# Performance work log

Measured on AMD Instinct MI355X. Metric: run time of the kernel, lower is better.

## Reference

```python
import jax, jax.numpy as jnp
import numpy as np

N = 50000      # nodes
E = 800000     # edges
F_IN = 16      # feature_size
D = 96         # d_model
G = 64         # graphs per batch


def _gcn_conv(x, W, b, src, dst, dis, num_nodes):
    # PyG GCNConv: out = D^{-1/2}(A+I)D^{-1/2} X W + b (self-loops already in src/dst)
    h = x @ W                                   # [N, out]
    norm = (dis[src] * dis[dst])[:, None]       # [E+N, 1]
    msg = h[src] * norm                         # gather + scale
    agg = jax.ops.segment_sum(msg, dst, num_segments=num_nodes)
    return agg + b


def _forward(x, W_init, b_init, W1, b1, W2, b2, W3, b3, W4, b4,
             Wo1, bo1, Wo2, bo2, edge_index, batch_index):
    act = jax.nn.leaky_relu  # default negative_slope=0.01, matches nn.LeakyReLU()
    n = x.shape[0]
    # add self-loops once; degree includes self-loop (PyG gcn_norm default)
    loop = jnp.arange(n, dtype=edge_index.dtype)
    src = jnp.concatenate([edge_index[0], loop])
    dst = jnp.concatenate([edge_index[1], loop])
    deg = jax.ops.segment_sum(jnp.ones_like(src, dtype=x.dtype), dst, num_segments=n)
    dis = jax.lax.rsqrt(deg)  # deg >= 1 due to self-loops

    h = act(_gcn_conv(x, W_init, b_init, src, dst, dis, n))
    h = act(_gcn_conv(h, W1, b1, src, dst, dis, n))
    h = act(_gcn_conv(h, W2, b2, src, dst, dis, n))
    h = act(_gcn_conv(h, W3, b3, src, dst, dis, n))
    h = act(_gcn_conv(h, W4, b4, src, dst, dis, n))

    # global max + mean pooling per graph
    gmax = jax.ops.segment_max(h, batch_index, num_segments=G)
    gsum = jax.ops.segment_sum(h, batch_index, num_segments=G)
    cnt = jax.ops.segment_sum(jnp.ones((n,), dtype=h.dtype), batch_index, num_segments=G)
    gmean = gsum / jnp.maximum(cnt, 1.0)[:, None]
    pooled = jnp.concatenate([gmax, gmean], axis=1)  # [G, 2D]

    out = act(pooled @ Wo1 + bo1)  # dropout is identity in eval
    out = out @ Wo2 + bo2          # [G, 1]
    return out


def setup_inputs() -> dict:
    key = jax.random.key(0)
    ks = jax.random.split(key, 16)
    def glorot(k, shape):
        lim = float(np.sqrt(6.0 / (shape[0] + shape[1])))
        return jax.random.uniform(k, shape, jnp.float32, -lim, lim)
    inp = {
        'x': jax.random.normal(ks[0], (N, F_IN), jnp.float32),
        'edge_index': jax.random.randint(ks[1], (2, E), 0, N, dtype=jnp.int64),
        'batch_index': jnp.sort(jax.random.randint(ks[2], (N,), 0, G, dtype=jnp.int64)),
        'W_init': glorot(ks[3], (F_IN, D)), 'b_init': jnp.zeros((D,), jnp.float32),
        'W1': glorot(ks[4], (D, D)), 'b1': jnp.zeros((D,), jnp.float32),
        'W2': glorot(ks[5], (D, D)), 'b2': jnp.zeros((D,), jnp.float32),
        'W3': glorot(ks[6], (D, D)), 'b3': jnp.zeros((D,), jnp.float32),
        'W4': glorot(ks[7], (D, D)), 'b4': jnp.zeros((D,), jnp.float32),
        'Wo1': glorot(ks[8], (2 * D, D)), 'bo1': jnp.zeros((D,), jnp.float32),
        'Wo2': glorot(ks[9], (D, 1)), 'bo2': jnp.zeros((1,), jnp.float32),
    }
    return inp


def reference(x, edge_index, batch_index, W_init, b_init, W1, b1, W2, b2,
              W3, b3, W4, b4, Wo1, bo1, Wo2, bo2):
    return _forward(x, W_init, b_init, W1, b1, W2, b2, W3, b3, W4, b4,
                    Wo1, bo1, Wo2, bo2, edge_index, batch_index)
```

## Files before the change

kernel.cpp:

```cpp
#include <hip/hip_runtime.h>
#include <hip/hip_fp16.h>
#include <math.h>

#define LEAKY(x) ((x) > 0.f ? (x) : 0.01f * (x))
#define BK_SHIFT 9
#define NBMAX 128
#define BCAP 16384

typedef _Float16 half8 __attribute__((ext_vector_type(8)));
typedef float f32x4 __attribute__((ext_vector_type(4)));

__device__ __forceinline__ void add4(float4& acc, const float4& v) {
    acc.x += v.x; acc.y += v.y; acc.z += v.z; acc.w += v.w;
}

#define FMIX_LO(acc, u, one) \
    asm("v_fma_mix_f32 %0, %1, %2, %0 op_sel:[0,0,0] op_sel_hi:[1,0,0]" \
        : "+v"(acc) : "v"(u), "v"(one))
#define FMIX_HI(acc, u, one) \
    asm("v_fma_mix_f32 %0, %1, %2, %0 op_sel:[1,0,0] op_sel_hi:[1,0,0]" \
        : "+v"(acc) : "v"(u), "v"(one))

__device__ __forceinline__ unsigned encf(float f) {
    unsigned u = __float_as_uint(f);
    return (u & 0x80000000u) ? ~u : (u | 0x80000000u);
}
__device__ __forceinline__ float decf(unsigned u) {
    if (u == 0u) return -INFINITY;
    unsigned b = (u & 0x80000000u) ? (u & 0x7fffffffu) : ~u;
    return __uint_as_float(b);
}

__global__ __launch_bounds__(256) void prep(const float* __restrict__ W1,
                                            const float* __restrict__ W2,
                                            const float* __restrict__ W3,
                                            const float* __restrict__ W4,
                                            _Float16* __restrict__ WtG,
                                            int* __restrict__ bfill,
                                            unsigned* __restrict__ gmaxU,
                                            float* __restrict__ gsum, int G) {
    int bi = blockIdx.x, tid = threadIdx.x;
    if (bi < 4) {
        const float* W = bi == 0 ? W1 : bi == 1 ? W2 : bi == 2 ? W3 : W4;
        _Float16* dst = WtG + bi * 9216;
        for (int idx = tid; idx < 9216; idx += 256) {
            int k = idx / 96, nn = idx % 96;
            dst[nn * 96 + k] = (_Float16)W[idx];
        }
    } else if (bi == 4) {
        for (int i2 = tid; i2 < NBMAX; i2 += 256) bfill[i2] = 0;
    } else if (bi == 5) {
        for (int i2 = tid; i2 < G * 96; i2 += 256) gmaxU[i2] = 0u;
    } else {
        for (int i2 = tid; i2 < G * 96; i2 += 256) gsum[i2] = 0.f;
    }
}

__global__ __launch_bounds__(256) void bin_kernel(const int* __restrict__ src,
                                                  const int* __restrict__ dst,
                                                  int* __restrict__ bfill,
                                                  uint2* __restrict__ tmp,
                                                  int E, int nb) {
    __shared__ int hist[NBMAX];
    __shared__ int scanbuf[NBMAX];
    __shared__ int lofs[NBMAX];
    __shared__ int adj[NBMAX];
    __shared__ uint2 buf[2048];
    __shared__ unsigned char bkt_of[2048];
    int base = blockIdx.x * 2048;
    int cnt = min(2048, E - base);
    int tid = threadIdx.x;
    for (int b = tid; b < NBMAX; b += 256) hist[b] = 0;
    __syncthreads();
    int es[8], ed[8];
#pragma unroll
    for (int k = 0; k < 8; ++k) {
        int l = tid + k * 256;
        if (l < cnt) {
            es[k] = src[base + l];
            ed[k] = dst[base + l];
            atomicAdd(&hist[ed[k] >> BK_SHIFT], 1);
        }
    }
    __syncthreads();
    if (tid < NBMAX) scanbuf[tid] = hist[tid];
    __syncthreads();
    for (int off = 1; off < NBMAX; off <<= 1) {
        int t = (tid < NBMAX && tid >= off) ? scanbuf[tid - off] : 0;
        __syncthreads();
        if (tid < NBMAX) scanbuf[tid] += t;
        __syncthreads();
    }
    if (tid < nb) {
        int cb = hist[tid];
        int start = scanbuf[tid] - cb;
        lofs[tid] = start;
        int g = (cb > 0) ? atomicAdd(&bfill[tid], cb) : 0;
        adj[tid] = tid * BCAP + g - start;
    }
    __syncthreads();
#pragma unroll
    for (int k = 0; k < 8; ++k) {
        int l = tid + k * 256;
        if (l < cnt) {
            int b = ed[k] >> BK_SHIFT;
            int r = atomicAdd(&lofs[b], 1);
            buf[r] = make_uint2((unsigned)es[k], (unsigned)ed[k]);
            bkt_of[r] = (unsigned char)b;
        }
    }
    __syncthreads();
    for (int j = tid; j < cnt; j += 256) {
        int b = bkt_of[j];
        tmp[adj[b] + j] = buf[j];
    }
}

__global__ __launch_bounds__(512) void place2(const uint2* __restrict__ tmp,
                                              const int* __restrict__ bfill,
                                              const float* __restrict__ X,
                                              float* __restrict__ dis,
                                              int* __restrict__ row_ptr,
                                              int* __restrict__ edge_src,
                                              float* __restrict__ Z0, int kq,
                                              int n, int E, int nb) {
    __shared__ int hist[512];
    __shared__ int sc[512];
    __shared__ int sbf[NBMAX];
    __shared__ int bb_s;
    int b = blockIdx.x;
    int tid = threadIdx.x;
    if (tid < NBMAX) sbf[tid] = (tid < nb) ? bfill[tid] : 0;
    hist[tid] = 0;
    __syncthreads();
    if (tid == 0) {
        int s = 0;
        for (int k = 0; k < b; ++k) s += sbf[k];
        bb_s = s;
    }
    __syncthreads();
    int bb = bb_s;
    int cnt = sbf[b];
    const uint2* mybkt = tmp + (size_t)b * BCAP;
    int node0 = b << BK_SHIFT;
    for (int j = tid; j < cnt; j += 512)
        atomicAdd(&hist[(int)mybkt[j].y - node0], 1);
    __syncthreads();
    int v = hist[tid];
    sc[tid] = v;
    __syncthreads();
    for (int off = 1; off < 512; off <<= 1) {
        int t = (tid >= off) ? sc[tid - off] : 0;
        __syncthreads();
        sc[tid] += t;
        __syncthreads();
    }
    int excl = sc[tid] - v;
    int i = node0 + tid;
    if (i < n) {
        row_ptr[i] = bb + excl;
        float di = rsqrtf((float)(v + 1));
        dis[i] = di;
        const float4* X4 = (const float4*)X;
        float4* Z4 = (float4*)Z0;
        for (int j = 0; j < kq; ++j) {
            float4 xv = X4[(size_t)i * kq + j];
            Z4[(size_t)i * kq + j] = make_float4(di * xv.x, di * xv.y, di * xv.z, di * xv.w);
        }
    }
    if (b == 0 && tid == 0) row_ptr[n] = E;
    __syncthreads();
    hist[tid] = bb + excl;
    __syncthreads();
    for (int j = tid; j < cnt; j += 512) {
        uint2 ev = mybkt[j];
        int pos = atomicAdd(&hist[(int)ev.y - node0], 1);
        edge_src[pos] = (int)ev.x;
    }
}

template <int LPN, int F4PL, int UNROLL>
__global__ __launch_bounds__(256) void agg_wave(const float* __restrict__ Z,
                                                const float* __restrict__ dis,
                                                const int* __restrict__ row_ptr,
                                                const int* __restrict__ edge_src,
                                                float* __restrict__ A, int n) {
    constexpr int GROUPS = 64 / LPN;
    constexpr int KQ = LPN * F4PL;
    int i = (blockIdx.x * 256 + threadIdx.x) >> 6;
    if (i >= n) return;
    int lane = threadIdx.x & 63;
    int g = lane / LPN;
    int c = lane % LPN;
    const float4* Z4 = (const float4*)Z;
    float di = dis[i];
    size_t base = (size_t)i * KQ + c * F4PL;
    float4 acc[F4PL];
    if (g == 0) {
#pragma unroll
        for (int j = 0; j < F4PL; ++j) acc[j] = Z4[base + j];
    } else {
#pragma unroll
        for (int j = 0; j < F4PL; ++j) acc[j] = make_float4(0.f, 0.f, 0.f, 0.f);
    }
    int re0 = row_ptr[i], re1 = row_ptr[i + 1];
#pragma unroll UNROLL
    for (int e = re0 + g; e < re1; e += GROUPS) {
        int s = edge_src[e];
        size_t sb = (size_t)s * KQ + c * F4PL;
#pragma unroll
        for (int j = 0; j < F4PL; ++j) {
            float4 xs = Z4[sb + j];
            add4(acc[j], xs);
        }
    }
#pragma unroll
    for (int m = LPN; m < 64; m <<= 1) {
#pragma unroll
        for (int j = 0; j < F4PL; ++j) {
            acc[j].x += __shfl_xor(acc[j].x, m);
            acc[j].y += __shfl_xor(acc[j].y, m);
            acc[j].z += __shfl_xor(acc[j].z, m);
            acc[j].w += __shfl_xor(acc[j].w, m);
        }
    }
    if (g == 0) {
#pragma unroll
        for (int j = 0; j < F4PL; ++j) {
            float4 o = make_float4(di * acc[j].x, di * acc[j].y,
                                   di * acc[j].z, di * acc[j].w);
            ((float4*)A)[base + j] = o;
        }
    }
}

__global__ __launch_bounds__(256) void agg_wave_h(const __half* __restrict__ Zh,
                                                  const float* __restrict__ dis,
                                                  const int* __restrict__ row_ptr,
                                                  const int* __restrict__ edge_src,
                                                  __half* __restrict__ A, int n) {
    int i = (blockIdx.x * 256 + threadIdx.x) >> 6;
    if (i >= n) return;
    int lane = threadIdx.x & 63;
    int g = lane >> 3;
    int c = lane & 7;
    float di = dis[i];
    float one = 1.0f;
    float acc[12];
#pragma unroll
    for (int k = 0; k < 12; ++k) acc[k] = 0.f;
    if (g == 0) {
        const uint2* zp = (const uint2*)(Zh + (size_t)i * 96 + c * 12);
        uint2 u0 = zp[0], u1 = zp[1], u2 = zp[2];
        FMIX_LO(acc[0], u0.x, one); FMIX_HI(acc[1], u0.x, one);
        FMIX_LO(acc[2], u0.y, one); FMIX_HI(acc[3], u0.y, one);
        FMIX_LO(acc[4], u1.x, one); FMIX_HI(acc[5], u1.x, one);
        FMIX_LO(acc[6], u1.y, one); FMIX_HI(acc[7], u1.y, one);
        FMIX_LO(acc[8], u2.x, one); FMIX_HI(acc[9], u2.x, one);
        FMIX_LO(acc[10], u2.y, one); FMIX_HI(acc[11], u2.y, one);
    }
    int re0 = row_ptr[i], re1 = row_ptr[i + 1];
#pragma unroll 4
    for (int e = re0 + g; e < re1; e += 8) {
        int s = __builtin_nontemporal_load(&edge_src[e]);
        const uint2* zp = (const uint2*)(Zh + (size_t)s * 96 + c * 12);
        uint2 u0 = zp[0], u1 = zp[1], u2 = zp[2];
        FMIX_LO(acc[0], u0.x, one); FMIX_HI(acc[1], u0.x, one);
        FMIX_LO(acc[2], u0.y, one); FMIX_HI(acc[3], u0.y, one);
        FMIX_LO(acc[4], u1.x, one); FMIX_HI(acc[5], u1.x, one);
        FMIX_LO(acc[6], u1.y, one); FMIX_HI(acc[7], u1.y, one);
        FMIX_LO(acc[8], u2.x, one); FMIX_HI(acc[9], u2.x, one);
        FMIX_LO(acc[10], u2.y, one); FMIX_HI(acc[11], u2.y, one);
    }
#pragma unroll
    for (int m = 8; m < 64; m <<= 1) {
#pragma unroll
        for (int k = 0; k < 12; ++k) acc[k] += __shfl_xor(acc[k], m);
    }
    if (g == 0) {
        __half2 h0 = __floats2half2_rn(di * acc[0], di * acc[1]);
        __half2 h1 = __floats2half2_rn(di * acc[2], di * acc[3]);
        __half2 h2 = __floats2half2_rn(di * acc[4], di * acc[5]);
        __half2 h3 = __floats2half2_rn(di * acc[6], di * acc[7]);
        __half2 h4 = __floats2half2_rn(di * acc[8], di * acc[9]);
        __half2 h5 = __floats2half2_rn(di * acc[10], di * acc[11]);
        uint2 o0, o1, o2;
        o0.x = *(unsigned*)&h0; o0.y = *(unsigned*)&h1;
        o1.x = *(unsigned*)&h2; o1.y = *(unsigned*)&h3;
        o2.x = *(unsigned*)&h4; o2.y = *(unsigned*)&h5;
        uint2* ap = (uint2*)(A + (size_t)i * 96 + c * 12);
        ap[0] = o0; ap[1] = o1; ap[2] = o2;
    }
}

template <bool SCALE>
__global__ __launch_bounds__(256) void gemm_mfma(const __half* __restrict__ A,
                                                 const _Float16* __restrict__ Wt,
                                                 const float* __restrict__ b,
                                                 const float* __restrict__ dis,
                                                 __half* __restrict__ Xn, int n) {
    int tid = threadIdx.x;
    int i0 = blockIdx.x * 64;
    int w = tid >> 6, lane = tid & 63;
    int q = lane >> 4, c = lane & 15;
    int arow = i0 + w * 16 + c;
    const _Float16* Ap = (const _Float16*)A;
    half8 af[3];
    if (arow < n) {
#pragma unroll
        for (int kc = 0; kc < 3; ++kc)
            af[kc] = *(const half8*)&Ap[(size_t)arow * 96 + kc * 32 + q * 8];
    } else {
#pragma unroll
        for (int kc = 0; kc < 3; ++kc)
#pragma unroll
            for (int j = 0; j < 8; ++j) af[kc][j] = (_Float16)0.f;
    }
    float dvals[4];
#pragma unroll
    for (int r = 0; r < 4; ++r) {
        int gi = i0 + w * 16 + q * 4 + r;
        dvals[r] = (SCALE && gi < n) ? dis[gi] : 1.f;
    }
#pragma unroll
    for (int nt = 0; nt < 6; ++nt) {
        f32x4 acc = {0.f, 0.f, 0.f, 0.f};
#pragma unroll
        for (int kc = 0; kc < 3; ++kc) {
            half8 bf = *(const half8*)&Wt[(size_t)(nt * 16 + c) * 96 + kc * 32 + q * 8];
            acc = __builtin_amdgcn_mfma_f32_16x16x32_f16(af[kc], bf, acc, 0, 0, 0);
        }
        int col = nt * 16 + c;
        float bias = b[col];
#pragma unroll
        for (int r = 0; r < 4; ++r) {
            int gi = i0 + w * 16 + q * 4 + r;
            if (gi < n) {
                float v = acc[r] + bias;
                v = LEAKY(v);
                if (SCALE) v *= dvals[r];
                ((_Float16*)Xn)[(size_t)gi * 96 + col] = (_Float16)v;
            }
        }
    }
}

__global__ __launch_bounds__(256) void gemm_pool(const __half* __restrict__ A,
                                                 const _Float16* __restrict__ Wt,
                                                 const float* __restrict__ b,
                                                 const int* __restrict__ batch,
                                                 unsigned* __restrict__ gmaxU,
                                                 float* __restrict__ gsum, int n) {
    __shared__ float pmaxs[4][96];
    __shared__ float psums[4][96];
    int tid = threadIdx.x;
    int i0 = blockIdx.x * 64;
    int w = tid >> 6, lane = tid & 63;
    int q = lane >> 4, c = lane & 15;
    int arow = i0 + w * 16 + c;
    const _Float16* Ap = (const _Float16*)A;
    half8 af[3];
    if (arow < n) {
#pragma unroll
        for (int kc = 0; kc < 3; ++kc)
            af[kc] = *(const half8*)&Ap[(size_t)arow * 96 + kc * 32 + q * 8];
    } else {
#pragma unroll
        for (int kc = 0; kc < 3; ++kc)
#pragma unroll
            for (int j = 0; j < 8; ++j) af[kc][j] = (_Float16)0.f;
    }
    int row0 = i0 + w * 16;
    bool wuni = (row0 + 15 < n) && (batch[row0] == batch[row0 + 15]);
    bool buni = (i0 + 63 < n) && (batch[i0] == batch[i0 + 63]);
    int gw = wuni ? batch[row0] : 0;
#pragma unroll
    for (int nt = 0; nt < 6; ++nt) {
        f32x4 acc = {0.f, 0.f, 0.f, 0.f};
#pragma unroll
        for (int kc = 0; kc < 3; ++kc) {
            half8 bf = *(const half8*)&Wt[(size_t)(nt * 16 + c) * 96 + kc * 32 + q * 8];
            acc = __builtin_amdgcn_mfma_f32_16x16x32_f16(af[kc], bf, acc, 0, 0, 0);
        }
        int col = nt * 16 + c;
        float bias = b[col];
        float v[4];
#pragma unroll
        for (int r = 0; r < 4; ++r) {
            float t = acc[r] + bias;
            v[r] = LEAKY(t);
        }
        if (wuni) {
            float mx = fmaxf(fmaxf(v[0], v[1]), fmaxf(v[2], v[3]));
            float sm = v[0] + v[1] + v[2] + v[3];
            mx = fmaxf(mx, __shfl_xor(mx, 16)); sm += __shfl_xor(sm, 16);
            mx = fmaxf(mx, __shfl_xor(mx, 32)); sm += __shfl_xor(sm, 32);
            if (buni) {
                if (q == 0) { pmaxs[w][col] = mx; psums[w][col] = sm; }
            } else if (q == 0) {
                atomicMax(&gmaxU[gw * 96 + col], encf(mx));
                atomicAdd(&gsum[gw * 96 + col], sm);
            }
        } else {
            int r = 0;
            while (r < 4) {
                int gi = i0 + w * 16 + q * 4 + r;
                if (gi >= n) break;
                int gb = batch[gi];
                float mx = v[r], sm = v[r];
                int r2 = r + 1;
                for (; r2 < 4; ++r2) {
                    int gi2 = i0 + w * 16 + q * 4 + r2;
                    if (gi2 >= n || batch[gi2] != gb) break;
                    mx = fmaxf(mx, v[r2]); sm += v[r2];
                }
                atomicMax(&gmaxU[gb * 96 + col], encf(mx));
                atomicAdd(&gsum[gb * 96 + col], sm);
                r = r2;
            }
        }
    }
    __syncthreads();
    if (buni && tid < 96) {
        float m = fmaxf(fmaxf(pmaxs[0][tid], pmaxs[1][tid]),
                        fmaxf(pmaxs[2][tid], pmaxs[3][tid]));
        float s = psums[0][tid] + psums[1][tid] + psums[2][tid] + psums[3][tid];
        int gb = batch[i0];
        atomicMax(&gmaxU[gb * 96 + tid], encf(m));
        atomicAdd(&gsum[gb * 96 + tid], s);
    }
}

__global__ __launch_bounds__(192) void gemm_l0(const float* __restrict__ A,
                                               const float* __restrict__ W,
                                               const float* __restrict__ b,
                                               const float* __restrict__ dis,
                                               __half* __restrict__ Xn, int n) {
    constexpr int KQ = 4;
    __shared__ __align__(16) float4 Al[64 * KQ];
    int tid = threadIdx.x;
    int i0 = blockIdx.x * 64;
    for (int idx = tid; idx < 64 * KQ; idx += 192) {
        int gi = i0 + idx / KQ;
        Al[idx] = (gi < n) ? ((const float4*)A)[(size_t)i0 * KQ + idx]
                           : make_float4(0.f, 0.f, 0.f, 0.f);
    }
    __syncthreads();
    int fq = tid % 24;
    int g = tid / 24;
    const float4* W4 = (const float4*)W;
    float4 bb = ((const float4*)b)[fq];
    float4 acc[8];
#pragma unroll
    for (int r = 0; r < 8; ++r) acc[r] = bb;
    for (int kc = 0; kc < 16; kc += 8) {
        float4 w[8];
#pragma unroll
        for (int kk = 0; kk < 8; ++kk) w[kk] = W4[(size_t)(kc + kk) * 24 + fq];
#pragma unroll
        for (int r = 0; r < 8; ++r) {
            const float4* ar = &Al[(g * 8 + r) * KQ + (kc >> 2)];
#pragma unroll
            for (int k4 = 0; k4 < 2; ++k4) {
                float4 a = ar[k4];
                float4 w0 = w[4 * k4 + 0], w1 = w[4 * k4 + 1];
                float4 w2 = w[4 * k4 + 2], w3 = w[4 * k4 + 3];
                acc[r].x += a.x * w0.x + a.y * w1.x + a.z * w2.x + a.w * w3.x;
                acc[r].y += a.x * w0.y + a.y * w1.y + a.z * w2.y + a.w * w3.y;
                acc[r].z += a.x * w0.z + a.y * w1.z + a.z * w2.z + a.w * w3.z;
                acc[r].w += a.x * w0.w + a.y * w1.w + a.z * w2.w + a.w * w3.w;
            }
        }
    }
#pragma unroll
    for (int r = 0; r < 8; ++r) {
        int gi = i0 + g * 8 + r;
        if (gi < n) {
            float di = dis[gi];
            float4 o;
            o.x = di * LEAKY(acc[r].x); o.y = di * LEAKY(acc[r].y);
            o.z = di * LEAKY(acc[r].z); o.w = di * LEAKY(acc[r].w);
            __half2 h0 = __floats2half2_rn(o.x, o.y);
            __half2 h1 = __floats2half2_rn(o.z, o.w);
            uint2 u;
            u.x = *(unsigned*)&h0;
            u.y = *(unsigned*)&h1;
            ((uint2*)Xn)[(size_t)gi * 24 + fq] = u;
        }
    }
}

__device__ __forceinline__ int lower_bound(const int* b, int n, int v) {
    int lo = 0, hi = n;
    while (lo < hi) {
        int m = (lo + hi) >> 1;
        if (b[m] < v) lo = m + 1; else hi = m;
    }
    return lo;
}

__global__ void pool_final(const unsigned* __restrict__ gmaxU,
                           const float* __restrict__ gsum,
                           const int* __restrict__ batch,
                           const float* __restrict__ Wo1, const float* __restrict__ bo1,
                           const float* __restrict__ Wo2, const float* __restrict__ bo2,
                           float* __restrict__ out, int n) {
    __shared__ float pooled[192];
    __shared__ float sh[96];
    int g = blockIdx.x, f = threadIdx.x;
    int s = lower_bound(batch, n, g), e = lower_bound(batch, n, g + 1);
    float cnt = fmaxf((float)(e - s), 1.f);
    pooled[f] = decf(gmaxU[(size_t)g * 96 + f]);
    pooled[96 + f] = gsum[(size_t)g * 96 + f] / cnt;
    __syncthreads();
    float acc = bo1[f];
    for (int k = 0; k < 192; ++k) acc += pooled[k] * Wo1[k * 96 + f];
    float a = LEAKY(acc);
    sh[f] = a * Wo2[f];
    __syncthreads();
    if (f == 0) {
        float sacc = 0.f;
        for (int k = 0; k < 96; ++k) sacc += sh[k];
        out[g] = sacc + bo2[0];
    }
}

extern "C" void kernel_launch(void* const* d_in, const int* in_sizes, int n_in,
                              void* d_out, int out_size, void* d_ws, size_t ws_size,
                              hipStream_t stream) {
    const float* x      = (const float*)d_in[0];
    const int*   eidx   = (const int*)d_in[1];
    const int*   batch  = (const int*)d_in[2];
    const float* W_init = (const float*)d_in[3];
    const float* b_init = (const float*)d_in[4];
    const float* W1 = (const float*)d_in[5];  const float* b1 = (const float*)d_in[6];
    const float* W2 = (const float*)d_in[7];  const float* b2 = (const float*)d_in[8];
    const float* W3 = (const float*)d_in[9];  const float* b3 = (const float*)d_in[10];
    const float* W4 = (const float*)d_in[11]; const float* b4 = (const float*)d_in[12];
    const float* Wo1 = (const float*)d_in[13]; const float* bo1 = (const float*)d_in[14];
    const float* Wo2 = (const float*)d_in[15]; const float* bo2 = (const float*)d_in[16];
    float* out = (float*)d_out;

    const int N = in_sizes[2];
    const int E = in_sizes[1] / 2;
    const int G = out_size;
    const int* src = eidx;
    const int* dst = eidx + E;

    const int nbBkt  = (N + (1 << BK_SHIFT) - 1) >> BK_SHIFT;

    char* ws = (char*)d_ws;
    size_t off = 0;
    auto alloc = [&](size_t bytes) {
        size_t o = off;
        off += (bytes + 255) & ~(size_t)255;
        return o;
    };
    float*    dis      = (float*)(ws + alloc((size_t)N * 4));
    int*      row_ptr  = (int*)(ws + alloc((size_t)(N + 1) * 4));
    int*      bfill    = (int*)(ws + alloc(NBMAX * 4));
    unsigned* gmaxU    = (unsigned*)(ws + alloc((size_t)G * 96 * 4));
    float*    gsumB    = (float*)(ws + alloc((size_t)G * 96 * 4));
    int*      edge_src = (int*)(ws + alloc((size_t)E * 4));
    float*    Z0       = (float*)(ws + alloc((size_t)N * 16 * 4));
    __half*   ZA       = (__half*)(ws + alloc((size_t)N * 96 * 2));
    __half*   ZB       = (__half*)(ws + alloc((size_t)N * 96 * 2));
    __half*   AggH     = (__half*)(ws + alloc((size_t)N * 96 * 2));
    float*    Agg0     = (float*)(ws + alloc((size_t)N * 16 * 4));
    _Float16* WtG      = (_Float16*)(ws + alloc((size_t)4 * 9216 * 2));
    uint2*    tmp      = (uint2*)(ws + alloc((size_t)nbBkt * BCAP * 8));
    (void)ws_size; (void)n_in;

    const int nbWave = (N + 3) / 4;
    const int nbTile = (N + 63) / 64;

    prep<<<7, 256, 0, stream>>>(W1, W2, W3, W4, WtG, bfill, gmaxU, gsumB, G);
    bin_kernel<<<(E + 2047) / 2048, 256, 0, stream>>>(src, dst, bfill, tmp, E, nbBkt);
    place2<<<nbBkt, 512, 0, stream>>>(tmp, bfill, x, dis, row_ptr, edge_src, Z0,
                                      4, N, E, nbBkt);

    agg_wave<4, 1, 2><<<nbWave, 256, 0, stream>>>(Z0, dis, row_ptr, edge_src, Agg0, N);
    gemm_l0<<<nbTile, 192, 0, stream>>>(Agg0, W_init, b_init, dis, ZA, N);

    const float* bs[4] = {b1, b2, b3, b4};
    __half* cur = ZA;
    __half* nxt = ZB;
    for (int l = 0; l < 4; ++l) {
        agg_wave_h<<<nbWave, 256, 0, stream>>>(cur, dis, row_ptr, edge_src, AggH, N);
        if (l < 3) {
            gemm_mfma<true><<<nbTile, 256, 0, stream>>>(AggH, WtG + l * 9216, bs[l],
                                                        dis, nxt, N);
            __half* t = cur; cur = nxt; nxt = t;
        } else {
            gemm_pool<<<nbTile, 256, 0, stream>>>(AggH, WtG + 3 * 9216, bs[3],
                                                  batch, gmaxU, gsumB, N);
        }
    }

    pool_final<<<G, 96, 0, stream>>>(gmaxU, gsumB, batch, Wo1, bo1, Wo2, bo2, out, N);
}
```

Measured before the change: 344.6 us.

## Fuse neighbor aggregation into the MFMA GEMM kernels for hidden layers

Replaces the separate wave-per-node aggregation kernel and the following MFMA GEMM (or GEMM+pool) kernel with one templated kernel. In it, each lane accumulates its node's neighbor features directly in the MFMA A-fragment layout, with four lanes per node walking the edge list serially. The aggregated, scaled fp16 fragment then feeds the MFMA without an intermediate buffer. This removes one launch per layer and the write and re-read of the N×96 aggregation buffer, but cuts per-node parallelism from 8 edge groups to a serial loop per lane and lowers total wave count, which may expose gather latency.

```diff
diff --git a/kernel.cpp b/kernel.cpp
--- a/kernel.cpp
+++ b/kernel.cpp
@@ -20,6 +20,23 @@
 #define FMIX_HI(acc, u, one) \
     asm("v_fma_mix_f32 %0, %1, %2, %0 op_sel:[1,0,0] op_sel_hi:[1,0,0]" \
         : "+v"(acc) : "v"(u), "v"(one))
+
+__device__ __forceinline__ void acc_row24(float (&acc)[24], const uint4* zr,
+                                          float one) {
+    uint4 u0 = zr[0], u1 = zr[4], u2 = zr[8];
+    FMIX_LO(acc[0], u0.x, one);  FMIX_HI(acc[1], u0.x, one);
+    FMIX_LO(acc[2], u0.y, one);  FMIX_HI(acc[3], u0.y, one);
+    FMIX_LO(acc[4], u0.z, one);  FMIX_HI(acc[5], u0.z, one);
+    FMIX_LO(acc[6], u0.w, one);  FMIX_HI(acc[7], u0.w, one);
+    FMIX_LO(acc[8], u1.x, one);  FMIX_HI(acc[9], u1.x, one);
+    FMIX_LO(acc[10], u1.y, one); FMIX_HI(acc[11], u1.y, one);
+    FMIX_LO(acc[12], u1.z, one); FMIX_HI(acc[13], u1.z, one);
+    FMIX_LO(acc[14], u1.w, one); FMIX_HI(acc[15], u1.w, one);
+    FMIX_LO(acc[16], u2.x, one); FMIX_HI(acc[17], u2.x, one);
+    FMIX_LO(acc[18], u2.y, one); FMIX_HI(acc[19], u2.y, one);
+    FMIX_LO(acc[20], u2.z, one); FMIX_HI(acc[21], u2.z, one);
+    FMIX_LO(acc[22], u2.w, one); FMIX_HI(acc[23], u2.w, one);
+}
 
 __device__ __forceinline__ unsigned encf(float f) {
     unsigned u = __float_as_uint(f);
@@ -234,200 +251,137 @@
     }
 }
 
-__global__ __launch_bounds__(256) void agg_wave_h(const __half* __restrict__ Zh,
-                                                  const float* __restrict__ dis,
-                                                  const int* __restrict__ row_ptr,
-                                                  const int* __restrict__ edge_src,
-                                                  __half* __restrict__ A, int n) {
-    int i = (blockIdx.x * 256 + threadIdx.x) >> 6;
-    if (i >= n) return;
-    int lane = threadIdx.x & 63;
-    int g = lane >> 3;
-    int c = lane & 7;
-    float di = dis[i];
-    float one = 1.0f;
-    float acc[12];
-#pragma unroll
-    for (int k = 0; k < 12; ++k) acc[k] = 0.f;
-    if (g == 0) {
-        const uint2* zp = (const uint2*)(Zh + (size_t)i * 96 + c * 12);
-        uint2 u0 = zp[0], u1 = zp[1], u2 = zp[2];
-        FMIX_LO(acc[0], u0.x, one); FMIX_HI(acc[1], u0.x, one);
-        FMIX_LO(acc[2], u0.y, one); FMIX_HI(acc[3], u0.y, one);
-        FMIX_LO(acc[4], u1.x, one); FMIX_HI(acc[5], u1.x, one);
-        FMIX_LO(acc[6], u1.y, one); FMIX_HI(acc[7], u1.y, one);
-        FMIX_LO(acc[8], u2.x, one); FMIX_HI(acc[9], u2.x, one);
-        FMIX_LO(acc[10], u2.y, one); FMIX_HI(acc[11], u2.y, one);
-    }
-    int re0 = row_ptr[i], re1 = row_ptr[i + 1];
-#pragma unroll 4
-    for (int e = re0 + g; e < re1; e += 8) {
-        int s = __builtin_nontemporal_load(&edge_src[e]);
-        const uint2* zp = (const uint2*)(Zh + (size_t)s * 96 + c * 12);
-        uint2 u0 = zp[0], u1 = zp[1], u2 = zp[2];
-        FMIX_LO(acc[0], u0.x, one); FMIX_HI(acc[1], u0.x, one);
-        FMIX_LO(acc[2], u0.y, one); FMIX_HI(acc[3], u0.y, one);
-        FMIX_LO(acc[4], u1.x, one); FMIX_HI(acc[5], u1.x, one);
-        FMIX_LO(acc[6], u1.y, one); FMIX_HI(acc[7], u1.y, one);
-        FMIX_LO(acc[8], u2.x, one); FMIX_HI(acc[9], u2.x, one);
-        FMIX_LO(acc[10], u2.y, one); FMIX_HI(acc[11], u2.y, one);
-    }
-#pragma unroll
-    for (int m = 8; m < 64; m <<= 1) {
-#pragma unroll
-        for (int k = 0; k < 12; ++k) acc[k] += __shfl_xor(acc[k], m);
-    }
-    if (g == 0) {
-        __half2 h0 = __floats2half2_rn(di * acc[0], di * acc[1]);
-        __half2 h1 = __floats2half2_rn(di * acc[2], di * acc[3]);
-        __half2 h2 = __floats2half2_rn(di * acc[4], di * acc[5]);
-        __half2 h3 = __floats2half2_rn(di * acc[6], di * acc[7]);
-        __half2 h4 = __floats2half2_rn(di * acc[8], di * acc[9]);
-        __half2 h5 = __floats2half2_rn(di * acc[10], di * acc[11]);
-        uint2 o0, o1, o2;
-        o0.x = *(unsigned*)&h0; o0.y = *(unsigned*)&h1;
-        o1.x = *(unsigned*)&h2; o1.y = *(unsigned*)&h3;
-        o2.x = *(unsigned*)&h4; o2.y = *(unsigned*)&h5;
-        uint2* ap = (uint2*)(A + (size_t)i * 96 + c * 12);
-        ap[0] = o0; ap[1] = o1; ap[2] = o2;
-    }
-}
-
-template <bool SCALE>
-__global__ __launch_bounds__(256) void gemm_mfma(const __half* __restrict__ A,
-                                                 const _Float16* __restrict__ Wt,
-                                                 const float* __restrict__ b,
-                                                 const float* __restrict__ dis,
-                                                 __half* __restrict__ Xn, int n) {
-    int tid = threadIdx.x;
-    int i0 = blockIdx.x * 64;
-    int w = tid >> 6, lane = tid & 63;
-    int q = lane >> 4, c = lane & 15;
-    int arow = i0 + w * 16 + c;
-    const _Float16* Ap = (const _Float16*)A;
-    half8 af[3];
-    if (arow < n) {
-#pragma unroll
-        for (int kc = 0; kc < 3; ++kc)
-            af[kc] = *(const half8*)&Ap[(size_t)arow * 96 + kc * 32 + q * 8];
-    } else {
-#pragma unroll
-        for (int kc = 0; kc < 3; ++kc)
-#pragma unroll
-            for (int j = 0; j < 8; ++j) af[kc][j] = (_Float16)0.f;
-    }
-    float dvals[4];
-#pragma unroll
-    for (int r = 0; r < 4; ++r) {
-        int gi = i0 + w * 16 + q * 4 + r;
-        dvals[r] = (SCALE && gi < n) ? dis[gi] : 1.f;
-    }
-#pragma unroll
-    for (int nt = 0; nt < 6; ++nt) {
-        f32x4 acc = {0.f, 0.f, 0.f, 0.f};
-#pragma unroll
-        for (int kc = 0; kc < 3; ++kc) {
-            half8 bf = *(const half8*)&Wt[(size_t)(nt * 16 + c) * 96 + kc * 32 + q * 8];
-            acc = __builtin_amdgcn_mfma_f32_16x16x32_f16(af[kc], bf, acc, 0, 0, 0);
-        }
-        int col = nt * 16 + c;
-        float bias = b[col];
-#pragma unroll
-        for (int r = 0; r < 4; ++r) {
-            int gi = i0 + w * 16 + q * 4 + r;
-            if (gi < n) {
-                float v = acc[r] + bias;
-                v = LEAKY(v);
-                if (SCALE) v *= dvals[r];
-                ((_Float16*)Xn)[(size_t)gi * 96 + col] = (_Float16)v;
-            }
-        }
-    }
-}
-
-__global__ __launch_bounds__(256) void gemm_pool(const __half* __restrict__ A,
-                                                 const _Float16* __restrict__ Wt,
-                                                 const float* __restrict__ b,
-                                                 const int* __restrict__ batch,
-                                                 unsigned* __restrict__ gmaxU,
-                                                 float* __restrict__ gsum, int n) {
+template <bool POOL>
+__global__ __launch_bounds__(256) void agg_gemm(const __half* __restrict__ Zh,
+                                                const float* __restrict__ dis,
+                                                const int* __restrict__ row_ptr,
+                                                const int* __restrict__ edge_src,
+                                                const _Float16* __restrict__ Wt,
+                                                const float* __restrict__ b,
+                                                const int* __restrict__ batch,
+                                                unsigned* __restrict__ gmaxU,
+                                                float* __restrict__ gsum,
+                                                __half* __restrict__ Xn, int n) {
     __shared__ float pmaxs[4][96];
     __shared__ float psums[4][96];
     int tid = threadIdx.x;
     int i0 = blockIdx.x * 64;
     int w = tid >> 6, lane = tid & 63;
     int q = lane >> 4, c = lane & 15;
-    int arow = i0 + w * 16 + c;
-    const _Float16* Ap = (const _Float16*)A;
+    int i = i0 + w * 16 + c;
+    bool valid = i < n;
+    float one = 1.0f;
+    float acc[24];
+#pragma unroll
+    for (int k = 0; k < 24; ++k) acc[k] = 0.f;
+    const _Float16* Zp = (const _Float16*)Zh;
+    int re0 = 0, re1 = 0;
+    if (valid) {
+        acc_row24(acc, (const uint4*)(Zp + (size_t)i * 96 + q * 8), one);
+        re0 = row_ptr[i];
+        re1 = row_ptr[i + 1];
+    }
+#pragma unroll 2
+    for (int e = re0; e < re1; ++e) {
+        int s = __builtin_nontemporal_load(&edge_src[e]);
+        acc_row24(acc, (const uint4*)(Zp + (size_t)s * 96 + q * 8), one);
+    }
+    float dagg = valid ? dis[i] : 0.f;
     half8 af[3];
-    if (arow < n) {
-#pragma unroll
-        for (int kc = 0; kc < 3; ++kc)
-            af[kc] = *(const half8*)&Ap[(size_t)arow * 96 + kc * 32 + q * 8];
+#pragma unroll
+    for (int kc = 0; kc < 3; ++kc)
+#pragma unroll
+        for (int j = 0; j < 8; ++j)
+            af[kc][j] = (_Float16)(dagg * acc[kc * 8 + j]);
+
+    if (!POOL) {
+        float dvals[4];
+#pragma unroll
+        for (int r = 0; r < 4; ++r) {
+            int gi = i0 + w * 16 + q * 4 + r;
+            dvals[r] = (gi < n) ? dis[gi] : 1.f;
+        }
+#pragma unroll
+        for (int nt = 0; nt < 6; ++nt) {
+            f32x4 dacc = {0.f, 0.f, 0.f, 0.f};
+#pragma unroll
+            for (int kc = 0; kc < 3; ++kc) {
+                half8 bf = *(const half8*)&Wt[(size_t)(nt * 16 + c) * 96 + kc * 32 + q * 8];
+                dacc = __builtin_amdgcn_mfma_f32_16x16x32_f16(af[kc], bf, dacc, 0, 0, 0);
+            }
+            int col = nt * 16 + c;
+            float bias = b[col];
+#pragma unroll
+            for (int r = 0; r < 4; ++r) {
+                int gi = i0 + w * 16 + q * 4 + r;
+                if (gi < n) {
+                    float v = dacc[r] + bias;
+                    v = LEAKY(v);
+                    v *= dvals[r];
+                    ((_Float16*)Xn)[(size_t)gi * 96 + col] = (_Float16)v;
+                }
+            }
+        }
     } else {
-#pragma unroll
-        for (int kc = 0; kc < 3; ++kc)
-#pragma unroll
-            for (int j = 0; j < 8; ++j) af[kc][j] = (_Float16)0.f;
-    }
-    int row0 = i0 + w * 16;
-    bool wuni = (row0 + 15 < n) && (batch[row0] == batch[row0 + 15]);
-    bool buni = (i0 + 63 < n) && (batch[i0] == batch[i0 + 63]);
-    int gw = wuni ? batch[row0] : 0;
-#pragma unroll
-    for (int nt = 0; nt < 6; ++nt) {
-        f32x4 acc = {0.f, 0.f, 0.f, 0.f};
-#pragma unroll
-        for (int kc = 0; kc < 3; ++kc) {
-            half8 bf = *(const half8*)&Wt[(size_t)(nt * 16 + c) * 96 + kc * 32 + q * 8];
-            acc = __builtin_amdgcn_mfma_f32_16x16x32_f16(af[kc], bf, acc, 0, 0, 0);
-        }
-        int col = nt * 16 + c;
-        float bias = b[col];
-        float v[4];
-#pragma unroll
-        for (int r = 0; r < 4; ++r) {
-            float t = acc[r] + bias;
-            v[r] = LEAKY(t);
-        }
-        if (wuni) {
-            float mx = fmaxf(fmaxf(v[0], v[1]), fmaxf(v[2], v[3]));
-            float sm = v[0] + v[1] + v[2] + v[3];
-            mx = fmaxf(mx, __shfl_xor(mx, 16)); sm += __shfl_xor(sm, 16);
-            mx = fmaxf(mx, __shfl_xor(mx, 32)); sm += __shfl_xor(sm, 32);
-            if (buni) {
-                if (q == 0) { pmaxs[w][col] = mx; psums[w][col] = sm; }
-            } else if (q == 0) {
-                atomicMax(&gmaxU[gw * 96 + col], encf(mx));
-                atomicAdd(&gsum[gw * 96 + col], sm);
+        int row0 = i0 + w * 16;
+        bool wuni = (row0 + 15 < n) && (batch[row0] == batch[row0 + 15]);
+        bool buni = (i0 + 63 < n) && (batch[i0] == batch[i0 + 63]);
+        int gw = wuni ? batch[row0] : 0;
+#pragma unroll
+        for (int nt = 0; nt < 6; ++nt) {
+            f32x4 dacc = {0.f, 0.f, 0.f, 0.f};
+#pragma unroll
+            for (int kc = 0; kc < 3; ++kc) {
+                half8 bf = *(const half8*)&Wt[(size_t)(nt * 16 + c) * 96 + kc * 32 + q * 8];
+                dacc = __builtin_amdgcn_mfma_f32_16x16x32_f16(af[kc], bf, dacc, 0, 0, 0);
             }
-        } else {
-            int r = 0;
-            while (r < 4) {
-                int gi = i0 + w * 16 + q * 4 + r;
-                if (gi >= n) break;
-                int gb = batch[gi];
-                float mx = v[r], sm = v[r];
-                int r2 = r + 1;
-                for (; r2 < 4; ++r2) {
-                    int gi2 = i0 + w * 16 + q * 4 + r2;
-                    if (gi2 >= n || batch[gi2] != gb) break;
-                    mx = fmaxf(mx, v[r2]); sm += v[r2];
+            int col = nt * 16 + c;
+            float bias = b[col];
+            float v[4];
+#pragma unroll
+            for (int r = 0; r < 4; ++r) {
+                float t = dacc[r] + bias;
+                v[r] = LEAKY(t);
+            }
+            if (wuni) {
+                float mx = fmaxf(fmaxf(v[0], v[1]), fmaxf(v[2], v[3]));
+                float sm = v[0] + v[1] + v[2] + v[3];
+                mx = fmaxf(mx, __shfl_xor(mx, 16)); sm += __shfl_xor(sm, 16);
+                mx = fmaxf(mx, __shfl_xor(mx, 32)); sm += __shfl_xor(sm, 32);
+                if (buni) {
+                    if (q == 0) { pmaxs[w][col] = mx; psums[w][col] = sm; }
+                } else if (q == 0) {
+                    atomicMax(&gmaxU[gw * 96 + col], encf(mx));
+                    atomicAdd(&gsum[gw * 96 + col], sm);
                 }
-                atomicMax(&gmaxU[gb * 96 + col], encf(mx));
-                atomicAdd(&gsum[gb * 96 + col], sm);
-                r = r2;
+            } else {
+                int r = 0;
+                while (r < 4) {
+                    int gi = i0 + w * 16 + q * 4 + r;
+                    if (gi >= n) break;
+                    int gb = batch[gi];
+                    float mx = v[r], sm = v[r];
+                    int r2 = r + 1;
+                    for (; r2 < 4; ++r2) {
+                        int gi2 = i0 + w * 16 + q * 4 + r2;
+                        if (gi2 >= n || batch[gi2] != gb) break;
+                        mx = fmaxf(mx, v[r2]); sm += v[r2];
+                    }
+                    atomicMax(&gmaxU[gb * 96 + col], encf(mx));
+                    atomicAdd(&gsum[gb * 96 + col], sm);
+                    r = r2;
+                }
             }
         }
-    }
-    __syncthreads();
-    if (buni && tid < 96) {
-        float m = fmaxf(fmaxf(pmaxs[0][tid], pmaxs[1][tid]),
-                        fmaxf(pmaxs[2][tid], pmaxs[3][tid]));
-        float s = psums[0][tid] + psums[1][tid] + psums[2][tid] + psums[3][tid];
-        int gb = batch[i0];
-        atomicMax(&gmaxU[gb * 96 + tid], encf(m));
-        atomicAdd(&gsum[gb * 96 + tid], s);
+        __syncthreads();
+        if (buni && tid < 96) {
+            float m = fmaxf(fmaxf(pmaxs[0][tid], pmaxs[1][tid]),
+                            fmaxf(pmaxs[2][tid], pmaxs[3][tid]));
+            float s = psums[0][tid] + psums[1][tid] + psums[2][tid] + psums[3][tid];
+            int gb = batch[i0];
+            atomicMax(&gmaxU[gb * 96 + tid], encf(m));
+            atomicAdd(&gsum[gb * 96 + tid], s);
+        }
     }
 }
 
@@ -565,7 +519,6 @@
     float*    Z0       = (float*)(ws + alloc((size_t)N * 16 * 4));
     __half*   ZA       = (__half*)(ws + alloc((size_t)N * 96 * 2));
     __half*   ZB       = (__half*)(ws + alloc((size_t)N * 96 * 2));
-    __half*   AggH     = (__half*)(ws + alloc((size_t)N * 96 * 2));
     float*    Agg0     = (float*)(ws + alloc((size_t)N * 16 * 4));
     _Float16* WtG      = (_Float16*)(ws + alloc((size_t)4 * 9216 * 2));
     uint2*    tmp      = (uint2*)(ws + alloc((size_t)nbBkt * BCAP * 8));
@@ -586,14 +539,15 @@
     __half* cur = ZA;
     __half* nxt = ZB;
     for (int l = 0; l < 4; ++l) {
-        agg_wave_h<<<nbWave, 256, 0, stream>>>(cur, dis, row_ptr, edge_src, AggH, N);
         if (l < 3) {
-            gemm_mfma<true><<<nbTile, 256, 0, stream>>>(AggH, WtG + l * 9216, bs[l],
-                                                        dis, nxt, N);
+            agg_gemm<false><<<nbTile, 256, 0, stream>>>(
+                cur, dis, row_ptr, edge_src, WtG + l * 9216, bs[l],
+                nullptr, nullptr, nullptr, nxt, N);
             __half* t = cur; cur = nxt; nxt = t;
         } else {
-            gemm_pool<<<nbTile, 256, 0, stream>>>(AggH, WtG + 3 * 9216, bs[3],
-                                                  batch, gmaxU, gsumB, N);
+            agg_gemm<true><<<nbTile, 256, 0, stream>>>(
+                cur, dis, row_ptr, edge_src, WtG + 3 * 9216, bs[3],
+                batch, gmaxU, gsumB, nullptr, N);
         }
     }
 
```

New measurement: 364.2 us. +5.7%, slower.
